# Kernel optimization log

Hardware: AMD Instinct MI355X
Metric: run time of the kernel (lower is better)

Reference implementation:

```python
import jax, jax.numpy as jnp
import numpy as np

B, N, D, H, FF, K, L = 8, 4096, 128, 8, 512, 16, 2
DH = D // H
EPS = 1e-5


def setup_inputs() -> dict:
    key = jax.random.key(0)
    ks = jax.random.split(key, 32)
    s = 0.02
    inp = {
        "x": jax.random.normal(ks[0], (B, N, 8), dtype=jnp.float32),
        "xyz_w": jax.random.normal(ks[1], (D, 3), jnp.float32) * s,
        "xyz_b": jnp.zeros((D,), jnp.float32),
        "ohe_w": jax.random.normal(ks[2], (D, 5), jnp.float32) * s,
        "ohe_b": jnp.zeros((D,), jnp.float32),
        # per-layer transformer params stacked on leading L axis
        "in_proj_w": jax.random.normal(ks[3], (L, 3 * D, D), jnp.float32) * s,
        "in_proj_b": jnp.zeros((L, 3 * D), jnp.float32),
        "out_proj_w": jax.random.normal(ks[4], (L, D, D), jnp.float32) * s,
        "out_proj_b": jnp.zeros((L, D), jnp.float32),
        "ln1_w": jnp.ones((L, D), jnp.float32),
        "ln1_b": jnp.zeros((L, D), jnp.float32),
        "lin1_w": jax.random.normal(ks[5], (L, FF, D), jnp.float32) * s,
        "lin1_b": jnp.zeros((L, FF), jnp.float32),
        "lin2_w": jax.random.normal(ks[6], (L, D, FF), jnp.float32) * s,
        "lin2_b": jnp.zeros((L, D), jnp.float32),
        "ln2_w": jnp.ones((L, D), jnp.float32),
        "ln2_b": jnp.zeros((L, D), jnp.float32),
        "fc1_w": jax.random.normal(ks[7], (FF, D), jnp.float32) * s,
        "fc1_b": jnp.zeros((FF,), jnp.float32),
        "fc2_w": jax.random.normal(ks[8], (1, FF), jnp.float32) * s,
        "fc2_b": jnp.zeros((1,), jnp.float32),
    }
    return inp


def _layer_norm(x, w, b):
    m = jnp.mean(x, -1, keepdims=True)
    v = jnp.mean((x - m) ** 2, -1, keepdims=True)
    return (x - m) * jax.lax.rsqrt(v + EPS) * w + b


def _knn_attention(xyz, feat):
    # squared euclidean distances preserve top-k ordering of cdist(p=2)
    d2 = jnp.sum((xyz[:, :, None, :] - xyz[:, None, :, :]) ** 2, -1)  # [B,N,N]
    _, idx = jax.lax.top_k(-d2, K + 1)  # ascending distance
    idx = idx[..., 1:]  # drop self -> [B,N,K]
    knn = jax.vmap(lambda f, i: f[i])(feat, idx)  # [B,N,K,D]
    scale = 1.0 / np.sqrt(D)
    scores = jnp.einsum('bnd,bnkd->bnk', feat, knn) * scale
    w = jax.nn.softmax(scores, -1)
    return jnp.einsum('bnk,bnkd->bnd', w, knn)


def _mha(x, in_w, in_b, out_w, out_b):
    qkv = x @ in_w.T + in_b  # [B,N,3D]
    q, k, v = jnp.split(qkv, 3, axis=-1)
    def heads(t):
        return t.reshape(B, N, H, DH).transpose(0, 2, 1, 3)  # [B,H,N,DH]
    q, k, v = heads(q), heads(k), heads(v)
    scores = jnp.einsum('bhqd,bhkd->bhqk', q, k) / np.sqrt(DH)
    a = jax.nn.softmax(scores, -1)
    o = jnp.einsum('bhqk,bhkd->bhqd', a, v).transpose(0, 2, 1, 3).reshape(B, N, D)
    return o @ out_w.T + out_b


def reference(x, xyz_w, xyz_b, ohe_w, ohe_b, in_proj_w, in_proj_b, out_proj_w,
              out_proj_b, ln1_w, ln1_b, lin1_w, lin1_b, lin2_w, lin2_b,
              ln2_w, ln2_b, fc1_w, fc1_b, fc2_w, fc2_b):
    xyz = x[:, :, :3]
    ohe = x[:, :, 3:8]
    feat = (xyz @ xyz_w.T + xyz_b) + (ohe @ ohe_w.T + ohe_b)  # [B,N,D]
    h = _knn_attention(xyz, feat)
    # post-norm TransformerEncoder (PyTorch default, relu, no dropout at eval)
    for l in range(L):
        a = _mha(h, in_proj_w[l], in_proj_b[l], out_proj_w[l], out_proj_b[l])
        h = _layer_norm(h + a, ln1_w[l], ln1_b[l])
        f = jax.nn.relu(h @ lin1_w[l].T + lin1_b[l]) @ lin2_w[l].T + lin2_b[l]
        h = _layer_norm(h + f, ln2_w[l], ln2_b[l])
    pooled = jnp.mean(h, axis=1)  # [B,D]
    out = jax.nn.sigmoid(jax.nn.relu(pooled @ fc1_w.T + fc1_b) @ fc2_w.T + fc2_b)
    return out
```

## Files before the change

### kernel.cpp

```cpp
#include <hip/hip_runtime.h>

#define Bq 8
#define Nq 4096
#define Dq 128
#define Hq 8
#define FFq 512
#define KNNq 16
#define Lq 2
#define DHq 16
#define EPSq 1e-5f

typedef _Float16 half4 __attribute__((ext_vector_type(4)));
typedef _Float16 half2t __attribute__((ext_vector_type(2)));
typedef float v4f __attribute__((ext_vector_type(4)));

static __device__ __forceinline__ half2t pkrtz(float a, float b) {
    return __builtin_bit_cast(half2t, __builtin_amdgcn_cvt_pkrtz(a, b));
}

__global__ __launch_bounds__(256) void prep_kernel(const float* __restrict__ x,
                                                   const float* __restrict__ xyz_w,
                                                   const float* __restrict__ xyz_b,
                                                   const float* __restrict__ ohe_w,
                                                   const float* __restrict__ ohe_b,
                                                   _Float16* __restrict__ feat16,
                                                   const float* __restrict__ ipw,
                                                   const float* __restrict__ opw,
                                                   const float* __restrict__ l1w,
                                                   const float* __restrict__ l2w,
                                                   _Float16* __restrict__ wb) {
    int bid = blockIdx.x;
    if (bid < 16384) {
        int i = bid * 256 + threadIdx.x;
        int d = i & 127;
        int t = i >> 7;
        const float* xr = x + (size_t)t * 8;
        float s = xyz_b[d] + ohe_b[d];
        s += xr[0] * xyz_w[d * 3 + 0] + xr[1] * xyz_w[d * 3 + 1] + xr[2] * xyz_w[d * 3 + 2];
        s += xr[3] * ohe_w[d * 5 + 0] + xr[4] * ohe_w[d * 5 + 1] + xr[5] * ohe_w[d * 5 + 2]
           + xr[6] * ohe_w[d * 5 + 3] + xr[7] * ohe_w[d * 5 + 4];
        feat16[i] = (_Float16)s;
    } else {
        int i = (bid - 16384) * 256 + threadIdx.x;
        float v;
        if (i < 98304) v = ipw[i];
        else if (i < 131072) v = opw[i - 98304];
        else if (i < 262144) v = l1w[i - 131072];
        else v = l2w[i - 262144];
        wb[i] = (_Float16)v;
    }
}

__global__ __launch_bounds__(512) void knn_kernel(const float* __restrict__ x, int* __restrict__ idx) {
    __shared__ __attribute__((aligned(16))) float sx[Nq];
    __shared__ __attribute__((aligned(16))) float sy[Nq];
    __shared__ __attribute__((aligned(16))) float sz[Nq];
    unsigned int (*md)[17] = (unsigned int (*)[17])sx;
    int b = blockIdx.y;
    int tid = threadIdx.x;
    for (int p = tid; p < Nq; p += 512) {
        const float* xr = x + ((size_t)b * Nq + p) * 8;
        sx[p] = xr[0]; sy[p] = xr[1]; sz[p] = xr[2];
    }
    __syncthreads();
    int qi = tid >> 3;
    int part = tid & 7;
    int n = blockIdx.x * 64 + qi;
    float qx = sx[n], qy = sy[n], qz = sz[n];
    unsigned int bdA[KNNq], bdB[KNNq];
#pragma unroll
    for (int i = 0; i < KNNq; i++) { bdA[i] = 0xFFFFFFFFu; bdB[i] = 0xFFFFFFFFu; }
    int j0 = part * 512;
    int rot = part;
    for (int jj = 0; jj < 256; jj++) {
        int j1 = j0 + ((jj + rot) & 511);
        int j2 = j0 + ((jj + 256 + rot) & 511);
        float p1x = sx[j1], p1y = sy[j1], p1z = sz[j1];
        float p2x = sx[j2], p2y = sy[j2], p2z = sz[j2];
        float dx1 = qx - p1x, dy1 = qy - p1y, dz1 = qz - p1z;
        float dx2 = qx - p2x, dy2 = qy - p2y, dz2 = qz - p2z;
        float d21 = fmaf(dx1, dx1, fmaf(dy1, dy1, dz1 * dz1));
        float d22 = fmaf(dx2, dx2, fmaf(dy2, dy2, dz2 * dz2));
        unsigned int k1 = (__float_as_uint(d21) & 0xFFFFF000u) | (unsigned int)j1;
        unsigned int k2 = (__float_as_uint(d22) & 0xFFFFF000u) | (unsigned int)j2;
        k1 = (j1 == n) ? 0xFFFFFFFFu : k1;
        k2 = (j2 == n) ? 0xFFFFFFFFu : k2;
#pragma unroll
        for (int i = 0; i < KNNq; i++) {
            unsigned int loA = bdA[i] < k1 ? bdA[i] : k1;
            unsigned int hiA = bdA[i] < k1 ? k1 : bdA[i];
            bdA[i] = loA; k1 = hiA;
            unsigned int loB = bdB[i] < k2 ? bdB[i] : k2;
            unsigned int hiB = bdB[i] < k2 ? k2 : bdB[i];
            bdB[i] = loB; k2 = hiB;
        }
    }
#pragma unroll
    for (int t = 0; t < KNNq; t++) {
        unsigned int key = bdB[t];
#pragma unroll
        for (int i = 0; i < KNNq; i++) {
            unsigned int lo = bdA[i] < key ? bdA[i] : key;
            unsigned int hi = bdA[i] < key ? key : bdA[i];
            bdA[i] = lo; key = hi;
        }
    }
    __syncthreads();
#pragma unroll
    for (int i = 0; i < KNNq; i++) md[tid][i] = bdA[i];
    __syncthreads();
    if (part == 0) {
        unsigned int pall = 0;
        int* op = idx + ((size_t)b * Nq + n) * KNNq;
        int base_row = qi * 8;
#pragma unroll
        for (int s = 0; s < KNNq; s++) {
            unsigned int best = 0xFFFFFFFFu; int bp = 0;
#pragma unroll
            for (int p2 = 0; p2 < 8; p2++) {
                unsigned int ptr = (pall >> (p2 * 4)) & 15u;
                unsigned int v = md[base_row + p2][ptr];
                if (v < best) { best = v; bp = p2; }
            }
            op[s] = (int)(best & 4095u);
            pall += (1u << (bp * 4));
        }
    }
}

__global__ __launch_bounds__(256, 4) void knn_attn_kernel(const _Float16* __restrict__ feat16,
                                                          const int* __restrict__ idx,
                                                          _Float16* __restrict__ h16) {
    int wave = threadIdx.x >> 6;
    int lane = threadIdx.x & 63;
    int token = blockIdx.x * 4 + wave;
    int b = token >> 12;
    half2t fh = ((const half2t*)(feat16 + (size_t)token * Dq))[lane];
    float2 f = make_float2((float)fh[0], (float)fh[1]);
    const int* ip = idx + (size_t)token * KNNq;
    int jj[KNNq];
#pragma unroll
    for (int k = 0; k < KNNq; k++) jj[k] = ip[k];
    float2 g[KNNq];
#pragma unroll
    for (int k = 0; k < KNNq; k++) {
        half2t gh = ((const half2t*)(feat16 + (((size_t)b << 12) + jj[k]) * Dq))[lane];
        g[k] = make_float2((float)gh[0], (float)gh[1]);
    }
    float sc[KNNq];
#pragma unroll
    for (int k = 0; k < KNNq; k++) {
        float p = f.x * g[k].x + f.y * g[k].y;
#pragma unroll
        for (int m = 1; m < 64; m <<= 1) p += __shfl_xor(p, m);
        sc[k] = p * 0.088388347648318447f;
    }
    float mx = sc[0];
#pragma unroll
    for (int k = 1; k < KNNq; k++) mx = fmaxf(mx, sc[k]);
    float sum = 0.f;
#pragma unroll
    for (int k = 0; k < KNNq; k++) { sc[k] = __expf(sc[k] - mx); sum += sc[k]; }
    float inv = 1.f / sum;
    float o0 = 0.f, o1 = 0.f;
#pragma unroll
    for (int k = 0; k < KNNq; k++) { o0 += sc[k] * g[k].x; o1 += sc[k] * g[k].y; }
    ((half2t*)(h16 + (size_t)token * Dq))[lane] = pkrtz(o0 * inv, o1 * inv);
}

template <int MODE>
__global__ __launch_bounds__(256) void hgemm_kernel(const _Float16* __restrict__ A,
                                                    const _Float16* __restrict__ W,
                                                    const float* __restrict__ bias,
                                                    void* __restrict__ Cout,
                                                    int M, int Nc, int K) {
    int tid = threadIdx.x;
    int lane = tid & 63, w = tid >> 6;
    int l15 = lane & 15, l4 = lane >> 4;
    int m0 = blockIdx.y * 64 + w * 16;
    int n0 = blockIdx.x * 64;
    const _Float16* Ap = A + (size_t)(m0 + l15) * K + l4 * 4;
    const _Float16* Wp = W + (size_t)(n0 + l15) * K + l4 * 4;
    v4f acc[4] = {{0.f, 0.f, 0.f, 0.f}, {0.f, 0.f, 0.f, 0.f}, {0.f, 0.f, 0.f, 0.f}, {0.f, 0.f, 0.f, 0.f}};
    for (int ks = 0; ks < K; ks += 16) {
        half4 af = *(const half4*)(Ap + ks);
#pragma unroll
        for (int nt = 0; nt < 4; nt++) {
            half4 wf = *(const half4*)(Wp + (size_t)nt * 16 * K + ks);
            acc[nt] = __builtin_amdgcn_mfma_f32_16x16x16f16(wf, af, acc[nt], 0, 0, 0);
        }
    }
    int m = m0 + l15;
#pragma unroll
    for (int nt = 0; nt < 4; nt++) {
        int nb = n0 + nt * 16 + l4 * 4;
        float4 bv = *(const float4*)(bias + nb);
        float v0 = acc[nt][0] + bv.x, v1 = acc[nt][1] + bv.y;
        float v2 = acc[nt][2] + bv.z, v3 = acc[nt][3] + bv.w;
        int n_base = n0 + nt * 16;
        int sel = n_base >> 7;
        if (MODE == 2 && sel == 0) {
            v0 *= 0.36067376f; v1 *= 0.36067376f; v2 *= 0.36067376f; v3 *= 0.36067376f;
        }
        half2t lo = pkrtz(v0, v1);
        half2t hi = pkrtz(v2, v3);
        half4 hv; hv[0] = lo[0]; hv[1] = lo[1]; hv[2] = hi[0]; hv[3] = hi[1];
        if (sel < 2) {
            int hh = (n_base >> 4) & 7;
            size_t base = (size_t)sel * (64ull * Nq * 16)
                        + ((size_t)((m >> 12) * 8 + hh)) * (Nq * 16)
                        + (size_t)(m & 4095) * 16 + l4 * 4;
            *(half4*)((_Float16*)Cout + base) = hv;
        } else {
            int hh = (n_base >> 4) & 7;
            size_t vb = 2ull * 64 * Nq * 16
                      + ((size_t)((m >> 12) * 8 + hh)) * (16 * Nq)
                      + (size_t)(m & 4095);
            _Float16* vp = (_Float16*)Cout + vb + (size_t)(l4 * 4) * Nq;
            vp[0 * Nq] = hv[0]; vp[1 * Nq] = hv[1]; vp[2 * Nq] = hv[2]; vp[3 * Nq] = hv[3];
        }
    }
}

__global__ __launch_bounds__(256) void flash12_kernel(const _Float16* __restrict__ pk,
                                                      _Float16* __restrict__ out16) {
    __shared__ _Float16 Ks[2][64 * 20];
    __shared__ _Float16 Vs[2][16 * 66];
    int tid = threadIdx.x;
    int lane = tid & 63, w = tid >> 6;
    int bh = blockIdx.y;
    const _Float16* Qb = pk + (size_t)bh * (Nq * 16);
    const _Float16* Kb = pk + (size_t)(64 + bh) * (Nq * 16);
    const _Float16* Vt = pk + 2ull * 64 * Nq * 16 + (size_t)bh * (16 * Nq);
    int q0 = blockIdx.x * 128 + w * 32;
    int l15 = lane & 15, l4 = lane >> 4;

    half4 qfA = *(const half4*)(Qb + (size_t)(q0 + l15) * 16 + l4 * 4);
    half4 qfB = *(const half4*)(Qb + (size_t)(q0 + 16 + l15) * 16 + l4 * 4);

    int sr = tid >> 2, sc = tid & 3;
    int vd = tid >> 4, vj = (tid & 15) * 4;
    const _Float16* Kg = Kb + (size_t)sr * 16 + sc * 4;
    const _Float16* Vg = Vt + (size_t)vd * Nq + vj;

    *(half4*)(Ks[0] + sr * 20 + sc * 4) = *(const half4*)(Kg);
    *(half4*)(Vs[0] + vd * 66 + vj) = *(const half4*)(Vg);
    __syncthreads();

    v4f oA = {0.f, 0.f, 0.f, 0.f}, oB = {0.f, 0.f, 0.f, 0.f};
    v4f lacA = {0.f, 0.f, 0.f, 0.f}, lacB = {0.f, 0.f, 0.f, 0.f};
    half4 ones;
    ones[0] = ones[1] = ones[2] = ones[3] = (_Float16)1.0f;

    for (int kt = 0; kt < Nq / 64; kt++) {
        int cur = kt & 1, nxt = cur ^ 1;
        if (kt < Nq / 64 - 1) {
            *(half4*)(Ks[nxt] + sr * 20 + sc * 4) = *(const half4*)(Kg + (size_t)(kt + 1) * 64 * 16);
            *(half4*)(Vs[nxt] + vd * 66 + vj) = *(const half4*)(Vg + (kt + 1) * 64);
        }
        half4 kf[4];
#pragma unroll
        for (int g = 0; g < 4; g++)
            kf[g] = *(const half4*)(Ks[cur] + (g * 16 + l15) * 20 + l4 * 4);
        v4f SA[4], SB[4];
#pragma unroll
        for (int g = 0; g < 4; g++) {
            SA[g] = __builtin_amdgcn_mfma_f32_16x16x16f16(kf[g], qfA, (v4f){0.f, 0.f, 0.f, 0.f}, 0, 0, 0);
            SB[g] = __builtin_amdgcn_mfma_f32_16x16x16f16(kf[g], qfB, (v4f){0.f, 0.f, 0.f, 0.f}, 0, 0, 0);
        }
        half4 PA[4], PB[4];
#pragma unroll
        for (int g = 0; g < 4; g++) {
            float a0 = __builtin_amdgcn_exp2f(SA[g][0]);
            float a1 = __builtin_amdgcn_exp2f(SA[g][1]);
            float a2 = __builtin_amdgcn_exp2f(SA[g][2]);
            float a3 = __builtin_amdgcn_exp2f(SA[g][3]);
            half2t alo = pkrtz(a0, a1);
            half2t ahi = pkrtz(a2, a3);
            PA[g][0] = alo[0]; PA[g][1] = alo[1]; PA[g][2] = ahi[0]; PA[g][3] = ahi[1];
            float b0 = __builtin_amdgcn_exp2f(SB[g][0]);
            float b1 = __builtin_amdgcn_exp2f(SB[g][1]);
            float b2 = __builtin_amdgcn_exp2f(SB[g][2]);
            float b3 = __builtin_amdgcn_exp2f(SB[g][3]);
            half2t blo = pkrtz(b0, b1);
            half2t bhi = pkrtz(b2, b3);
            PB[g][0] = blo[0]; PB[g][1] = blo[1]; PB[g][2] = bhi[0]; PB[g][3] = bhi[1];
        }
#pragma unroll
        for (int g = 0; g < 4; g++) {
            half4 vf = *(const half4*)(Vs[cur] + l15 * 66 + g * 16 + l4 * 4);
            lacA = __builtin_amdgcn_mfma_f32_16x16x16f16(ones, PA[g], lacA, 0, 0, 0);
            oA = __builtin_amdgcn_mfma_f32_16x16x16f16(vf, PA[g], oA, 0, 0, 0);
            lacB = __builtin_amdgcn_mfma_f32_16x16x16f16(ones, PB[g], lacB, 0, 0, 0);
            oB = __builtin_amdgcn_mfma_f32_16x16x16f16(vf, PB[g], oB, 0, 0, 0);
        }
        __syncthreads();
    }
    int b = bh >> 3, hh = bh & 7;
    {
        float inv = 1.f / lacA[0];
        int row = q0 + l15;
        half2t lo = pkrtz(oA[0] * inv, oA[1] * inv);
        half2t hi = pkrtz(oA[2] * inv, oA[3] * inv);
        half4 hv; hv[0] = lo[0]; hv[1] = lo[1]; hv[2] = hi[0]; hv[3] = hi[1];
        *(half4*)(out16 + ((size_t)(b * Nq + row)) * Dq + hh * 16 + l4 * 4) = hv;
    }
    {
        float inv = 1.f / lacB[0];
        int row = q0 + 16 + l15;
        half2t lo = pkrtz(oB[0] * inv, oB[1] * inv);
        half2t hi = pkrtz(oB[2] * inv, oB[3] * inv);
        half4 hv; hv[0] = lo[0]; hv[1] = lo[1]; hv[2] = hi[0]; hv[3] = hi[1];
        *(half4*)(out16 + ((size_t)(b * Nq + row)) * Dq + hh * 16 + l4 * 4) = hv;
    }
}

__global__ __launch_bounds__(256) void hgemm_ln_kernel(const _Float16* __restrict__ A,
                                                       const _Float16* __restrict__ W,
                                                       const float* __restrict__ bias,
                                                       const float* __restrict__ lnw,
                                                       const float* __restrict__ lnb,
                                                       _Float16* __restrict__ h16,
                                                       int K) {
    int tid = threadIdx.x;
    int lane = tid & 63, w = tid >> 6;
    int l15 = lane & 15, l4 = lane >> 4;
    int m0 = blockIdx.x * 64 + w * 16;
    const _Float16* Ap = A + (size_t)(m0 + l15) * K + l4 * 4;
    const _Float16* Wp = W + (size_t)l15 * K + l4 * 4;
    v4f acc[8] = {};
    for (int ks = 0; ks < K; ks += 16) {
        half4 af = *(const half4*)(Ap + ks);
#pragma unroll
        for (int nt = 0; nt < 8; nt++) {
            half4 wf = *(const half4*)(Wp + (size_t)nt * 16 * K + ks);
            acc[nt] = __builtin_amdgcn_mfma_f32_16x16x16f16(wf, af, acc[nt], 0, 0, 0);
        }
    }
    int m = m0 + l15;
    float x[8][4];
    float psum = 0.f;
#pragma unroll
    for (int nt = 0; nt < 8; nt++) {
        int nb = nt * 16 + l4 * 4;
        float4 bv = *(const float4*)(bias + nb);
        half4 rv = *(const half4*)(h16 + (size_t)m * Dq + nb);
        x[nt][0] = acc[nt][0] + bv.x + (float)rv[0];
        x[nt][1] = acc[nt][1] + bv.y + (float)rv[1];
        x[nt][2] = acc[nt][2] + bv.z + (float)rv[2];
        x[nt][3] = acc[nt][3] + bv.w + (float)rv[3];
        psum += (x[nt][0] + x[nt][1]) + (x[nt][2] + x[nt][3]);
    }
    psum += __shfl_xor(psum, 16);
    psum += __shfl_xor(psum, 32);
    float mean = psum * (1.f / 128.f);
    float vsum = 0.f;
#pragma unroll
    for (int nt = 0; nt < 8; nt++)
#pragma unroll
        for (int r = 0; r < 4; r++) {
            x[nt][r] -= mean;
            vsum += x[nt][r] * x[nt][r];
        }
    vsum += __shfl_xor(vsum, 16);
    vsum += __shfl_xor(vsum, 32);
    float inv = rsqrtf(vsum * (1.f / 128.f) + EPSq);
#pragma unroll
    for (int nt = 0; nt < 8; nt++) {
        int nb = nt * 16 + l4 * 4;
        float4 wv = *(const float4*)(lnw + nb);
        float4 bb = *(const float4*)(lnb + nb);
        float y0 = x[nt][0] * inv * wv.x + bb.x;
        float y1 = x[nt][1] * inv * wv.y + bb.y;
        float y2 = x[nt][2] * inv * wv.z + bb.z;
        float y3 = x[nt][3] * inv * wv.w + bb.w;
        half2t lo = pkrtz(y0, y1);
        half2t hi = pkrtz(y2, y3);
        half4 hv2; hv2[0] = lo[0]; hv2[1] = lo[1]; hv2[2] = hi[0]; hv2[3] = hi[1];
        *(half4*)(h16 + (size_t)m * Dq + nb) = hv2;
    }
}

template <int LAST>
__global__ __launch_bounds__(256) void ffn_kernel(const _Float16* __restrict__ h16in,
                                                  const _Float16* __restrict__ W1,
                                                  const float* __restrict__ b1,
                                                  const _Float16* __restrict__ W2,
                                                  const float* __restrict__ b2,
                                                  const float* __restrict__ lnw,
                                                  const float* __restrict__ lnb,
                                                  _Float16* __restrict__ h16,
                                                  float* __restrict__ part) {
    int tid = threadIdx.x;
    int lane = tid & 63, w = tid >> 6;
    int l15 = lane & 15, l4 = lane >> 4;
    int m0 = blockIdx.x * 64 + w * 16;
    int m = m0 + l15;
    const _Float16* Ap = h16in + (size_t)m * Dq + l4 * 4;
    half4 afr[8];
#pragma unroll
    for (int t = 0; t < 8; t++) afr[t] = *(const half4*)(Ap + t * 16);
    half4 mid[32];
#pragma unroll
    for (int c = 0; c < 8; c++) {
        v4f acc[4] = {};
#pragma unroll
        for (int t = 0; t < 8; t++) {
#pragma unroll
            for (int nt = 0; nt < 4; nt++) {
                half4 wf = *(const half4*)(W1 + (size_t)(c * 64 + nt * 16 + l15) * 128 + t * 16 + l4 * 4);
                acc[nt] = __builtin_amdgcn_mfma_f32_16x16x16f16(wf, afr[t], acc[nt], 0, 0, 0);
            }
        }
#pragma unroll
        for (int nt = 0; nt < 4; nt++) {
            float4 bv = *(const float4*)(b1 + c * 64 + nt * 16 + l4 * 4);
            float v0 = fmaxf(acc[nt][0] + bv.x, 0.f);
            float v1 = fmaxf(acc[nt][1] + bv.y, 0.f);
            float v2 = fmaxf(acc[nt][2] + bv.z, 0.f);
            float v3 = fmaxf(acc[nt][3] + bv.w, 0.f);
            half2t lo = pkrtz(v0, v1), hi = pkrtz(v2, v3);
            half4 hv; hv[0] = lo[0]; hv[1] = lo[1]; hv[2] = hi[0]; hv[3] = hi[1];
            mid[c * 4 + nt] = hv;
        }
    }
    v4f acc8[8] = {};
#pragma unroll 4
    for (int t = 0; t < 32; t++) {
#pragma unroll
        for (int nt = 0; nt < 8; nt++) {
            half4 wf = *(const half4*)(W2 + (size_t)(nt * 16 + l15) * 512 + t * 16 + l4 * 4);
            acc8[nt] = __builtin_amdgcn_mfma_f32_16x16x16f16(wf, mid[t], acc8[nt], 0, 0, 0);
        }
    }
    float x[8][4];
    float psum = 0.f;
#pragma unroll
    for (int nt = 0; nt < 8; nt++) {
        int nb = nt * 16 + l4 * 4;
        float4 bv = *(const float4*)(b2 + nb);
        x[nt][0] = acc8[nt][0] + bv.x + (float)afr[nt][0];
        x[nt][1] = acc8[nt][1] + bv.y + (float)afr[nt][1];
        x[nt][2] = acc8[nt][2] + bv.z + (float)afr[nt][2];
        x[nt][3] = acc8[nt][3] + bv.w + (float)afr[nt][3];
        psum += (x[nt][0] + x[nt][1]) + (x[nt][2] + x[nt][3]);
    }
    psum += __shfl_xor(psum, 16);
    psum += __shfl_xor(psum, 32);
    float mean = psum * (1.f / 128.f);
    float vsum = 0.f;
#pragma unroll
    for (int nt = 0; nt < 8; nt++)
#pragma unroll
        for (int r = 0; r < 4; r++) {
            x[nt][r] -= mean;
            vsum += x[nt][r] * x[nt][r];
        }
    vsum += __shfl_xor(vsum, 16);
    vsum += __shfl_xor(vsum, 32);
    float inv = rsqrtf(vsum * (1.f / 128.f) + EPSq);
#pragma unroll
    for (int nt = 0; nt < 8; nt++) {
        int nb = nt * 16 + l4 * 4;
        float4 wv = *(const float4*)(lnw + nb);
        float4 bb = *(const float4*)(lnb + nb);
        x[nt][0] = x[nt][0] * inv * wv.x + bb.x;
        x[nt][1] = x[nt][1] * inv * wv.y + bb.y;
        x[nt][2] = x[nt][2] * inv * wv.z + bb.z;
        x[nt][3] = x[nt][3] * inv * wv.w + bb.w;
        if (!LAST) {
            half2t lo = pkrtz(x[nt][0], x[nt][1]);
            half2t hi = pkrtz(x[nt][2], x[nt][3]);
            half4 hv2; hv2[0] = lo[0]; hv2[1] = lo[1]; hv2[2] = hi[0]; hv2[3] = hi[1];
            *(half4*)(h16 + (size_t)m * Dq + nb) = hv2;
        }
    }
    if (LAST) {
#pragma unroll
        for (int nt = 0; nt < 8; nt++)
#pragma unroll
            for (int r = 0; r < 4; r++) {
                float v = x[nt][r];
                v += __shfl_xor(v, 1);
                v += __shfl_xor(v, 2);
                v += __shfl_xor(v, 4);
                v += __shfl_xor(v, 8);
                x[nt][r] = v;
            }
        if (l15 == 0) {
            float* pp = part + ((size_t)blockIdx.x * 4 + w) * Dq;
#pragma unroll
            for (int nt = 0; nt < 8; nt++)
#pragma unroll
                for (int r = 0; r < 4; r++)
                    pp[nt * 16 + l4 * 4 + r] = x[nt][r];
        }
    }
}

__global__ __launch_bounds__(512) void head_kernel(const float* __restrict__ part,
                                                   const float* __restrict__ fc1_w, const float* __restrict__ fc1_b,
                                                   const float* __restrict__ fc2_w, const float* __restrict__ fc2_b,
                                                   float* __restrict__ out) {
    __shared__ float psh[Dq];
    __shared__ float red[512];
    int b = blockIdx.x, f = threadIdx.x;
    if (f < Dq) {
        float s = 0.f;
        for (int c = 0; c < 256; c++) s += part[((size_t)b * 256 + c) * Dq + f];
        psh[f] = s * (1.f / 4096.f);
    }
    __syncthreads();
    const float* wr = fc1_w + (size_t)f * Dq;
    float s = fc1_b[f];
    for (int d = 0; d < Dq; d++) s += psh[d] * wr[d];
    red[f] = fmaxf(s, 0.f) * fc2_w[f];
    __syncthreads();
    for (int st = 256; st > 0; st >>= 1) {
        if (f < st) red[f] += red[f + st];
        __syncthreads();
    }
    if (f == 0) out[b] = 1.f / (1.f + __expf(-(red[0] + fc2_b[0])));
}

extern "C" void kernel_launch(void* const* d_in, const int* in_sizes, int n_in,
                              void* d_out, int out_size, void* d_ws, size_t ws_size,
                              hipStream_t stream) {
    const float* x        = (const float*)d_in[0];
    const float* xyz_w    = (const float*)d_in[1];
    const float* xyz_b    = (const float*)d_in[2];
    const float* ohe_w    = (const float*)d_in[3];
    const float* ohe_b    = (const float*)d_in[4];
    const float* in_proj_w  = (const float*)d_in[5];
    const float* in_proj_b  = (const float*)d_in[6];
    const float* out_proj_w = (const float*)d_in[7];
    const float* out_proj_b = (const float*)d_in[8];
    const float* ln1_w    = (const float*)d_in[9];
    const float* ln1_b    = (const float*)d_in[10];
    const float* lin1_w   = (const float*)d_in[11];
    const float* lin1_b   = (const float*)d_in[12];
    const float* lin2_w   = (const float*)d_in[13];
    const float* lin2_b   = (const float*)d_in[14];
    const float* ln2_w    = (const float*)d_in[15];
    const float* ln2_b    = (const float*)d_in[16];
    const float* fc1_w    = (const float*)d_in[17];
    const float* fc1_b    = (const float*)d_in[18];
    const float* fc2_w    = (const float*)d_in[19];
    const float* fc2_b    = (const float*)d_in[20];
    float* outp = (float*)d_out;

    char* ws = (char*)d_ws;
    size_t off = 0;
    auto alloc = [&](size_t bytes) { void* p = ws + off; off += (bytes + 255) & ~255ULL; return p; };
    _Float16*  feat16 = (_Float16*)alloc((size_t)Bq * Nq * Dq * 2);
    _Float16*  h16    = (_Float16*)alloc((size_t)Bq * Nq * Dq * 2);
    _Float16*  abuf16 = (_Float16*)alloc((size_t)Bq * Nq * Dq * 2);
    _Float16*  pkb    = (_Float16*)alloc(3ull * 64 * Nq * 16 * 2);
    _Float16*  wb     = (_Float16*)alloc(393216ull * 2);
    int*       idx    = (int*)alloc((size_t)Bq * Nq * KNNq * 4);
    float*     part   = (float*)alloc(2048ull * Dq * 4);
    if (off > ws_size) return;

    const _Float16* wip16 = wb;
    const _Float16* wop16 = wb + 98304;
    const _Float16* wl116 = wb + 131072;
    const _Float16* wl216 = wb + 262144;

    int M = Bq * Nq;

    prep_kernel<<<16384 + 1536, 256, 0, stream>>>(x, xyz_w, xyz_b, ohe_w, ohe_b, feat16,
                                                  in_proj_w, out_proj_w, lin1_w, lin2_w, wb);
    knn_kernel<<<dim3(Nq / 64, Bq), 512, 0, stream>>>(x, idx);
    knn_attn_kernel<<<M / 4, 256, 0, stream>>>(feat16, idx, h16);

    for (int l = 0; l < Lq; l++) {
        hgemm_kernel<2><<<dim3(384 / 64, M / 64), 256, 0, stream>>>(
            h16, wip16 + (size_t)l * 384 * 128, in_proj_b + l * 384, pkb, M, 384, 128);
        flash12_kernel<<<dim3(Nq / 128, Bq * Hq), 256, 0, stream>>>(pkb, abuf16);
        hgemm_ln_kernel<<<M / 64, 256, 0, stream>>>(
            abuf16, wop16 + (size_t)l * 128 * 128, out_proj_b + l * 128,
            ln1_w + l * 128, ln1_b + l * 128, h16, 128);
        if (l == 0) {
            ffn_kernel<0><<<M / 64, 256, 0, stream>>>(
                h16, wl116, lin1_b, wl216, lin2_b, ln2_w, ln2_b, h16, part);
        } else {
            ffn_kernel<1><<<M / 64, 256, 0, stream>>>(
                h16, wl116 + (size_t)l * 512 * 128, lin1_b + l * 512,
                wl216 + (size_t)l * 128 * 512, lin2_b + l * 128,
                ln2_w + l * 128, ln2_b + l * 128, h16, part);
        }
    }

    head_kernel<<<Bq, 512, 0, stream>>>(part, fc1_w, fc1_b, fc2_w, fc2_b, outp);
}
```

Before: 1.107 ms.

## Replace per-element insertion top-k with batched bitonic sort and merge

The kNN selection loop used to insert each candidate distance key into two sorted 16-entry lists, one compare-swap chain per element. It now computes 16 candidate keys at a time, sorts them with a bitonic network, and merges them into the running top-16 with a min step plus a bitonic cleanup. This cuts the compare-swap count per candidate and removes the final merge of the two lists. In exchange it needs more live registers for the batch array.

```diff
diff --git a/kernel.cpp b/kernel.cpp
--- a/kernel.cpp
+++ b/kernel.cpp
@@ -67,47 +67,63 @@
     int part = tid & 7;
     int n = blockIdx.x * 64 + qi;
     float qx = sx[n], qy = sy[n], qz = sz[n];
-    unsigned int bdA[KNNq], bdB[KNNq];
-#pragma unroll
-    for (int i = 0; i < KNNq; i++) { bdA[i] = 0xFFFFFFFFu; bdB[i] = 0xFFFFFFFFu; }
+    unsigned int top[16];
+#pragma unroll
+    for (int i = 0; i < 16; i++) top[i] = 0xFFFFFFFFu;
     int j0 = part * 512;
     int rot = part;
-    for (int jj = 0; jj < 256; jj++) {
-        int j1 = j0 + ((jj + rot) & 511);
-        int j2 = j0 + ((jj + 256 + rot) & 511);
-        float p1x = sx[j1], p1y = sy[j1], p1z = sz[j1];
-        float p2x = sx[j2], p2y = sy[j2], p2z = sz[j2];
-        float dx1 = qx - p1x, dy1 = qy - p1y, dz1 = qz - p1z;
-        float dx2 = qx - p2x, dy2 = qy - p2y, dz2 = qz - p2z;
-        float d21 = fmaf(dx1, dx1, fmaf(dy1, dy1, dz1 * dz1));
-        float d22 = fmaf(dx2, dx2, fmaf(dy2, dy2, dz2 * dz2));
-        unsigned int k1 = (__float_as_uint(d21) & 0xFFFFF000u) | (unsigned int)j1;
-        unsigned int k2 = (__float_as_uint(d22) & 0xFFFFF000u) | (unsigned int)j2;
-        k1 = (j1 == n) ? 0xFFFFFFFFu : k1;
-        k2 = (j2 == n) ? 0xFFFFFFFFu : k2;
-#pragma unroll
-        for (int i = 0; i < KNNq; i++) {
-            unsigned int loA = bdA[i] < k1 ? bdA[i] : k1;
-            unsigned int hiA = bdA[i] < k1 ? k1 : bdA[i];
-            bdA[i] = loA; k1 = hiA;
-            unsigned int loB = bdB[i] < k2 ? bdB[i] : k2;
-            unsigned int hiB = bdB[i] < k2 ? k2 : bdB[i];
-            bdB[i] = loB; k2 = hiB;
-        }
-    }
-#pragma unroll
-    for (int t = 0; t < KNNq; t++) {
-        unsigned int key = bdB[t];
-#pragma unroll
-        for (int i = 0; i < KNNq; i++) {
-            unsigned int lo = bdA[i] < key ? bdA[i] : key;
-            unsigned int hi = bdA[i] < key ? key : bdA[i];
-            bdA[i] = lo; key = hi;
+    for (int bb = 0; bb < 32; bb++) {
+        unsigned int c[16];
+#pragma unroll
+        for (int u = 0; u < 16; u++) {
+            int j = j0 + ((bb * 16 + rot + u) & 511);
+            float px = sx[j], py = sy[j], pz = sz[j];
+            float dx = qx - px, dy = qy - py, dz = qz - pz;
+            float d2 = fmaf(dx, dx, fmaf(dy, dy, dz * dz));
+            unsigned int ky = (__float_as_uint(d2) & 0xFFFFF000u) | (unsigned int)j;
+            c[u] = (j == n) ? 0xFFFFFFFFu : ky;
+        }
+#pragma unroll
+        for (int kk = 2; kk <= 16; kk <<= 1) {
+#pragma unroll
+            for (int jj = 16 >> 1; jj > 0; jj >>= 1) {
+                if (jj < kk) {
+#pragma unroll
+                    for (int i = 0; i < 16; i++) {
+                        int l = i ^ jj;
+                        if (l > i) {
+                            unsigned int a0 = c[i], b0 = c[l];
+                            unsigned int mn = a0 < b0 ? a0 : b0;
+                            unsigned int mx = a0 < b0 ? b0 : a0;
+                            bool up = ((i & kk) == 0);
+                            c[i] = up ? mn : mx;
+                            c[l] = up ? mx : mn;
+                        }
+                    }
+                }
+            }
+        }
+#pragma unroll
+        for (int i = 0; i < 16; i++) {
+            unsigned int a0 = top[i], b0 = c[15 - i];
+            top[i] = a0 < b0 ? a0 : b0;
+        }
+#pragma unroll
+        for (int d = 8; d >= 1; d >>= 1) {
+#pragma unroll
+            for (int i = 0; i < 16; i++) {
+                if ((i & d) == 0) {
+                    int l = i | d;
+                    unsigned int a0 = top[i], b0 = top[l];
+                    top[i] = a0 < b0 ? a0 : b0;
+                    top[l] = a0 < b0 ? b0 : a0;
+                }
+            }
         }
     }
     __syncthreads();
 #pragma unroll
-    for (int i = 0; i < KNNq; i++) md[tid][i] = bdA[i];
+    for (int i = 0; i < 16; i++) md[tid][i] = top[i];
     __syncthreads();
     if (part == 0) {
         unsigned int pall = 0;
```

Result: faster. 1.018 ms (-8.0%).
